# Kernel tuning notes

Measured on AMD Instinct MI355X. Metric: run time of the kernel, lower is better.

Reference implementation:

```python
import jax, jax.numpy as jnp
import numpy as np

B, TQ, TK = 8, 2048, 4096
DIM_IMG, DIM_TXT, HS = 512, 128, 64


def _make_freqs(seqlen, half_dim):
    # standard RoPE angles: theta = pos * 10000^(-2i/d); stored as [T, half_dim, 2] = (cos, sin)
    inv = 1.0 / (10000.0 ** (np.arange(0, half_dim, dtype=np.float32) / half_dim))
    ang = np.arange(seqlen, dtype=np.float32)[:, None] * inv[None, :]
    return jnp.asarray(np.stack([np.cos(ang), np.sin(ang)], axis=-1))


def _rot_complex(x, f):
    # x: [B, T, D]; f: [T, D//2, 2] (real, imag). Complex multiply on (even, odd) pairs.
    xr = x.reshape(*x.shape[:-1], -1, 2)
    a, b = xr[..., 0], xr[..., 1]
    fr, fi = f[None, ..., 0], f[None, ..., 1]
    out = jnp.stack([a * fr - b * fi, a * fi + b * fr], axis=-1)
    return out.reshape(x.shape)


def _rot2d(x, fx, fy):
    vx, vy = jnp.split(x, 2, axis=-1)
    return jnp.concatenate([_rot_complex(vx, fx), _rot_complex(vy, fy)], axis=-1)


def setup_inputs() -> dict:
    key = jax.random.key(0)
    k1, k2, k3, k4, k5 = jax.random.split(key, 5)
    return {
        "x_image": jax.random.normal(k1, (B, TK, DIM_IMG), dtype=jnp.float32),
        "x_text_emb": jax.random.normal(k2, (B, TQ, DIM_TXT), dtype=jnp.float32),
        "x_latex_mask": jax.random.randint(k3, (B, TQ), 0, 2, dtype=jnp.int32),
        "freqs_latex": _make_freqs(TQ, HS // 2),
        "freqs_img_x": _make_freqs(TK, HS // 4),
        "freqs_img_y": _make_freqs(TK, HS // 4),
        "Wk": jax.random.normal(k4, (HS, DIM_IMG), dtype=jnp.float32) * (DIM_IMG ** -0.5),
        "Wq": jax.random.normal(k5, (HS, DIM_TXT), dtype=jnp.float32) * (DIM_TXT ** -0.5),
        "Wv": jax.random.normal(jax.random.fold_in(key, 7), (HS, DIM_IMG), dtype=jnp.float32) * (DIM_IMG ** -0.5),
    }


def reference(x_image, x_text_emb, x_latex_mask, freqs_latex, freqs_img_x, freqs_img_y, Wk, Wq, Wv):
    C = x_image.shape[-1]  # original divides by sqrt of image embed dim (512), not head_size
    k = jnp.einsum("btc,hc->bth", x_image, Wk)
    k = jax.lax.stop_gradient(_rot2d(k, freqs_img_x, freqs_img_y))  # torch.no_grad in source
    q = jnp.einsum("bsc,hc->bsh", x_text_emb, Wq)
    q = jax.lax.stop_gradient(_rot_complex(q, freqs_latex))  # torch.no_grad in source
    v = jnp.einsum("btc,hc->bth", x_image, Wv)
    wei = jnp.einsum("bsh,bth->bst", q, k) / (C ** 0.5)  # [B, TQ, TK]
    softwei = jax.nn.softmax(wei, axis=-1)
    out = jnp.einsum("bst,bth->bsh", softwei, v)
    return out
```

## Files before the change

### kernel.cpp

```cpp
#include <hip/hip_runtime.h>


#define B_    8
#define TQ_   2048
#define TK_   4096
#define DIMG  512
#define DTXT  128
#define HS_   64
#define NSPL  4
#define TSPL  (TK_ / NSPL)

typedef float f32x4 __attribute__((ext_vector_type(4)));
typedef __bf16 bf16x8 __attribute__((ext_vector_type(8)));

static __device__ __forceinline__ unsigned short f2bf(float x) {
    __bf16 b = (__bf16)x;
    return __builtin_bit_cast(unsigned short, b);
}
static __device__ __forceinline__ unsigned pk2(float a, float b) {
    return (unsigned)f2bf(a) | ((unsigned)f2bf(b) << 16);
}

#define STAGE_KV(XBUF, WBUF, kc)                                                      \
    {                                                                                 \
        _Pragma("unroll")                                                             \
        for (int m = 0; m < 4; ++m) {                                                 \
            int lin = tid + 256 * m;                                                  \
            int r = lin >> 4;                                                         \
            int c = (lin & 15) * 4;                                                   \
            float4 v = *(const float4*)(x_image + ((size_t)(b * TK_ + t0 + r)) * DIMG + (kc) + c); \
            *(uint2*)&XBUF[r][c] = make_uint2(pk2(v.x, v.y), pk2(v.z, v.w));          \
        }                                                                             \
        _Pragma("unroll")                                                             \
        for (int m = 0; m < 8; ++m) {                                                 \
            int lin = tid + 256 * m;                                                  \
            int r = lin >> 4;                                                         \
            int c = (lin & 15) * 4;                                                   \
            const float* src = (r < 64) ? (Wk + (size_t)r * DIMG + (kc) + c)          \
                                        : (Wv + (size_t)(r - 64) * DIMG + (kc) + c);  \
            float4 v = *(const float4*)src;                                           \
            *(uint2*)&WBUF[r][c] = make_uint2(pk2(v.x, v.y), pk2(v.z, v.w));          \
        }                                                                             \
    }

#define COMPUTE_KV(XBUF, WBUF)                                                        \
    {                                                                                 \
        bf16x8 a0 = *(const bf16x8*)&XBUF[16 * w + col][hi4 * 8];                     \
        bf16x8 a1 = *(const bf16x8*)&XBUF[16 * w + col][hi4 * 8 + 32];                \
        _Pragma("unroll")                                                             \
        for (int g = 0; g < 8; ++g) {                                                 \
            bf16x8 b0 = *(const bf16x8*)&WBUF[g * 16 + col][hi4 * 8];                 \
            bf16x8 b1 = *(const bf16x8*)&WBUF[g * 16 + col][hi4 * 8 + 32];            \
            acc[g] = __builtin_amdgcn_mfma_f32_16x16x32_bf16(a0, b0, acc[g], 0, 0, 0);\
            acc[g] = __builtin_amdgcn_mfma_f32_16x16x32_bf16(a1, b1, acc[g], 0, 0, 0);\
        }                                                                             \
    }

__global__ __launch_bounds__(256) void proj_fused_kernel(
    const float* __restrict__ x_image, const float* __restrict__ fx,
    const float* __restrict__ fy, const float* __restrict__ Wk,
    const float* __restrict__ Wv, const float* __restrict__ x_text,
    const float* __restrict__ fl, const float* __restrict__ Wq,
    unsigned short* __restrict__ K_ws, unsigned short* __restrict__ Vt_ws,
    unsigned short* __restrict__ Q_ws)
{
    __shared__ __align__(16) unsigned short lds[27648];

    const int tid = threadIdx.x;
    const int bid = blockIdx.x;
    const int w  = tid >> 6;
    const int l  = tid & 63;
    const int col = l & 15;
    const int hi4 = l >> 4;

    if (bid < 512) {
        auto Xc0 = (unsigned short(*)[72])(lds);
        auto Xc1 = (unsigned short(*)[72])(lds + 4608);
        auto Wc0 = (unsigned short(*)[72])(lds + 9216);
        auto Wc1 = (unsigned short(*)[72])(lds + 18432);

        const int b  = bid & 7;
        const int t0 = (bid >> 3) * 64;

        f32x4 acc[8];
        #pragma unroll
        for (int g = 0; g < 8; ++g) acc[g] = (f32x4){0.f, 0.f, 0.f, 0.f};

        STAGE_KV(Xc0, Wc0, 0);
        __syncthreads();
        for (int c2 = 0; c2 < 8; c2 += 2) {
            STAGE_KV(Xc1, Wc1, (c2 + 1) * 64);
            COMPUTE_KV(Xc0, Wc0);
            __syncthreads();
            if (c2 + 2 < 8) STAGE_KV(Xc0, Wc0, (c2 + 2) * 64);
            COMPUTE_KV(Xc1, Wc1);
            __syncthreads();
        }

        const int rbase = hi4 * 4;
        #pragma unroll
        for (int g = 0; g < 4; ++g) {
            int h = g * 16 + col;
            const float* ftab = (h < 32) ? fx : fy;
            int i = (h & 31) >> 1;
            float sgn = (h & 1) ? 1.f : -1.f;
            #pragma unroll
            for (int j = 0; j < 4; ++j) {
                int t = t0 + 16 * w + rbase + j;
                float v = acc[g][j];
                float p = __shfl_xor(v, 1);
                float2 cs = *(const float2*)(ftab + ((size_t)t * 16 + i) * 2);
                float o = v * cs.x + sgn * p * cs.y;
                K_ws[((size_t)(b * TK_ + t)) * HS_ + h] = f2bf(o);
            }
        }
        #pragma unroll
        for (int g = 4; g < 8; ++g) {
            int h = (g - 4) * 16 + col;
            int tb = t0 + 16 * w + rbase;
            *(uint2*)&Vt_ws[((size_t)(b * HS_ + h)) * TK_ + tb] =
                make_uint2(pk2(acc[g][0], acc[g][1]), pk2(acc[g][2], acc[g][3]));
        }
    } else {
        auto Xq = (unsigned short(*)[136])(lds);
        auto Wl = (unsigned short(*)[136])(lds + 8704);

        const int b  = bid & 7;
        const int s0 = ((bid - 512) >> 3) * 64;

        #pragma unroll
        for (int m = 0; m < 8; ++m) {
            int lin = tid + 256 * m;
            int r = lin >> 5;
            int c = (lin & 31) * 4;
            float4 v = *(const float4*)(x_text + ((size_t)(b * TQ_ + s0 + r)) * DTXT + c);
            *(uint2*)&Xq[r][c] = make_uint2(pk2(v.x, v.y), pk2(v.z, v.w));
        }
        #pragma unroll
        for (int m = 0; m < 8; ++m) {
            int lin = tid + 256 * m;
            int r = lin >> 5;
            int c = (lin & 31) * 4;
            float4 v = *(const float4*)(Wq + (size_t)r * DTXT + c);
            *(uint2*)&Wl[r][c] = make_uint2(pk2(v.x, v.y), pk2(v.z, v.w));
        }
        __syncthreads();

        f32x4 acc[4];
        #pragma unroll
        for (int g = 0; g < 4; ++g) acc[g] = (f32x4){0.f, 0.f, 0.f, 0.f};
        #pragma unroll
        for (int kk = 0; kk < 4; ++kk) {
            bf16x8 a = *(const bf16x8*)&Xq[16 * w + col][hi4 * 8 + kk * 32];
            #pragma unroll
            for (int g = 0; g < 4; ++g) {
                bf16x8 bb = *(const bf16x8*)&Wl[g * 16 + col][hi4 * 8 + kk * 32];
                acc[g] = __builtin_amdgcn_mfma_f32_16x16x32_bf16(a, bb, acc[g], 0, 0, 0);
            }
        }

        const float SCALE = 0.044194173824159216f;
        const int rbase = hi4 * 4;
        #pragma unroll
        for (int g = 0; g < 4; ++g) {
            int h = g * 16 + col;
            int i = h >> 1;
            float sgn = (h & 1) ? 1.f : -1.f;
            #pragma unroll
            for (int j = 0; j < 4; ++j) {
                int s = s0 + 16 * w + rbase + j;
                float v = acc[g][j];
                float p = __shfl_xor(v, 1);
                float2 cs = *(const float2*)(fl + ((size_t)s * 32 + i) * 2);
                float o = (v * cs.x + sgn * p * cs.y) * SCALE;
                Q_ws[((size_t)(b * TQ_ + s)) * HS_ + h] = f2bf(o);
            }
        }
    }
}

__global__ __launch_bounds__(512, 4) void attn_partial_kernel(
    const unsigned short* __restrict__ Q_ws,
    const unsigned short* __restrict__ K_ws,
    const unsigned short* __restrict__ Vt_ws,
    float* __restrict__ num_ws, float* __restrict__ den_ws)
{
    __shared__ unsigned short Kt[128][72];
    __shared__ unsigned short Vv[64][136];
    __shared__ unsigned short Pl[8][16][136];

    const int tid  = threadIdx.x;
    const int bid  = blockIdx.x;
    const int b    = bid & 7;
    const int rest = bid >> 3;
    const int stile = rest & 15;
    const int split = rest >> 4;
    const int s0 = stile * 128;
    const int w  = tid >> 6;
    const int l  = tid & 63;
    const int col = l & 15;
    const int hi4 = l >> 4;

    const int srow = s0 + 16 * w + col;
    bf16x8 q0 = *(const bf16x8*)(Q_ws + ((size_t)(b * TQ_ + srow)) * HS_ + hi4 * 8);
    bf16x8 q1 = *(const bf16x8*)(Q_ws + ((size_t)(b * TQ_ + srow)) * HS_ + hi4 * 8 + 32);

    f32x4 oacc[4];
    #pragma unroll
    for (int g = 0; g < 4; ++g) oacc[g] = (f32x4){0.f, 0.f, 0.f, 0.f};
    f32x4 den = (f32x4){0.f, 0.f, 0.f, 0.f};

    const int tbase = split * TSPL;
    const int lin1 = tid + 512;
    const int kr_r0 = tid >> 3,  kr_h0 = (tid & 7) * 8;
    const int kr_r1 = lin1 >> 3, kr_h1 = (lin1 & 7) * 8;
    const int vr_h0 = tid >> 4,  vr_t0 = (tid & 15) * 8;
    const int vr_h1 = lin1 >> 4, vr_t1 = (lin1 & 15) * 8;

    *(uint4*)&Kt[kr_r0][kr_h0] = *(const uint4*)(K_ws + ((size_t)(b * TK_ + tbase + kr_r0)) * HS_ + kr_h0);
    *(uint4*)&Kt[kr_r1][kr_h1] = *(const uint4*)(K_ws + ((size_t)(b * TK_ + tbase + kr_r1)) * HS_ + kr_h1);
    *(uint4*)&Vv[vr_h0][vr_t0] = *(const uint4*)(Vt_ws + ((size_t)(b * HS_ + vr_h0)) * TK_ + tbase + vr_t0);
    *(uint4*)&Vv[vr_h1][vr_t1] = *(const uint4*)(Vt_ws + ((size_t)(b * HS_ + vr_h1)) * TK_ + tbase + vr_t1);
    __syncthreads();

    for (int ti = 0; ti < TSPL / 128; ++ti) {
        const int tt = tbase + ti * 128;
        const bool pre = (ti + 1 < TSPL / 128);
        uint4 kr0, kr1, vr0, vr1;
        if (pre) {
            const int tn = tt + 128;
            kr0 = *(const uint4*)(K_ws + ((size_t)(b * TK_ + tn + kr_r0)) * HS_ + kr_h0);
            kr1 = *(const uint4*)(K_ws + ((size_t)(b * TK_ + tn + kr_r1)) * HS_ + kr_h1);
            vr0 = *(const uint4*)(Vt_ws + ((size_t)(b * HS_ + vr_h0)) * TK_ + tn + vr_t0);
            vr1 = *(const uint4*)(Vt_ws + ((size_t)(b * HS_ + vr_h1)) * TK_ + tn + vr_t1);
        }

        #pragma unroll
        for (int n = 0; n < 8; ++n) {
            bf16x8 k0 = *(const bf16x8*)&Kt[n * 16 + col][hi4 * 8];
            bf16x8 k1 = *(const bf16x8*)&Kt[n * 16 + col][hi4 * 8 + 32];
            f32x4 p = (f32x4){0.f, 0.f, 0.f, 0.f};
            p = __builtin_amdgcn_mfma_f32_16x16x32_bf16(q0, k0, p, 0, 0, 0);
            p = __builtin_amdgcn_mfma_f32_16x16x32_bf16(q1, k1, p, 0, 0, 0);
            #pragma unroll
            for (int j = 0; j < 4; ++j) {
                float e = __expf(p[j]);
                den[j] += e;
                Pl[w][hi4 * 4 + j][n * 16 + col] = f2bf(e);
            }
        }
        asm volatile("s_waitcnt lgkmcnt(0)" ::: "memory");
        __builtin_amdgcn_sched_barrier(0);

        #pragma unroll
        for (int c = 0; c < 4; ++c) {
            bf16x8 pa = *(const bf16x8*)&Pl[w][col][c * 32 + hi4 * 8];
            #pragma unroll
            for (int g = 0; g < 4; ++g) {
                bf16x8 vb = *(const bf16x8*)&Vv[g * 16 + col][c * 32 + hi4 * 8];
                oacc[g] = __builtin_amdgcn_mfma_f32_16x16x32_bf16(pa, vb, oacc[g], 0, 0, 0);
            }
        }
        __syncthreads();
        if (pre) {
            *(uint4*)&Kt[kr_r0][kr_h0] = kr0;
            *(uint4*)&Kt[kr_r1][kr_h1] = kr1;
            *(uint4*)&Vv[vr_h0][vr_t0] = vr0;
            *(uint4*)&Vv[vr_h1][vr_t1] = vr1;
        }
        __syncthreads();
    }

    #pragma unroll
    for (int m = 1; m < 16; m <<= 1) {
        #pragma unroll
        for (int j = 0; j < 4; ++j) den[j] += __shfl_xor(den[j], m);
    }

    const size_t sec = (size_t)(split * B_ + b) * TQ_;
    #pragma unroll
    for (int g = 0; g < 4; ++g) {
        #pragma unroll
        for (int j = 0; j < 4; ++j) {
            int s = s0 + 16 * w + hi4 * 4 + j;
            num_ws[(sec + s) * HS_ + g * 16 + col] = oacc[g][j];
        }
    }
    if (col == 0) {
        #pragma unroll
        for (int j = 0; j < 4; ++j) {
            int s = s0 + 16 * w + hi4 * 4 + j;
            den_ws[sec + s] = den[j];
        }
    }
}

__global__ __launch_bounds__(256) void attn_reduce_kernel(
    const float* __restrict__ num_ws, const float* __restrict__ den_ws,
    float* __restrict__ out)
{
    const int idx = blockIdx.x * 256 + threadIdx.x;
    const int row = idx >> 4;
    const size_t spl4 = (size_t)B_ * TQ_ * HS_ / 4;
    const float4* n4 = (const float4*)num_ws;
    float4 a = n4[idx];
    float4 v1 = n4[idx + spl4];
    float4 v2 = n4[idx + 2 * spl4];
    float4 v3 = n4[idx + 3 * spl4];
    a.x += v1.x + v2.x + v3.x;
    a.y += v1.y + v2.y + v3.y;
    a.z += v1.z + v2.z + v3.z;
    a.w += v1.w + v2.w + v3.w;
    float d = den_ws[row] + den_ws[row + B_ * TQ_] +
              den_ws[row + 2 * B_ * TQ_] + den_ws[row + 3 * B_ * TQ_];
    float inv = 1.f / d;
    a.x *= inv; a.y *= inv; a.z *= inv; a.w *= inv;
    ((float4*)out)[idx] = a;
}

__global__ __launch_bounds__(256) void attn_kernel(
    const unsigned short* __restrict__ Q_ws,
    const unsigned short* __restrict__ K_ws,
    const unsigned short* __restrict__ Vt_ws,
    float* __restrict__ out)
{
    __shared__ unsigned short Kt[128][72];
    __shared__ unsigned short Vv[64][136];
    __shared__ unsigned short Pl[4][16][136];

    const int tid = threadIdx.x;
    const int b  = blockIdx.x & 7;
    const int s0 = (blockIdx.x >> 3) * 64;
    const int w  = tid >> 6;
    const int l  = tid & 63;
    const int col = l & 15;
    const int hi4 = l >> 4;

    const int srow = s0 + 16 * w + col;
    bf16x8 q0 = *(const bf16x8*)(Q_ws + ((size_t)(b * TQ_ + srow)) * HS_ + hi4 * 8);
    bf16x8 q1 = *(const bf16x8*)(Q_ws + ((size_t)(b * TQ_ + srow)) * HS_ + hi4 * 8 + 32);

    f32x4 oacc[4];
    #pragma unroll
    for (int g = 0; g < 4; ++g) oacc[g] = (f32x4){0.f, 0.f, 0.f, 0.f};
    f32x4 den = (f32x4){0.f, 0.f, 0.f, 0.f};

    for (int tt = 0; tt < TK_; tt += 128) {
        #pragma unroll
        for (int m = 0; m < 4; ++m) {
            int lin = tid + 256 * m;
            int r = lin >> 3;
            int h = (lin & 7) * 8;
            *(uint4*)&Kt[r][h] = *(const uint4*)(K_ws + ((size_t)(b * TK_ + tt + r)) * HS_ + h);
        }
        #pragma unroll
        for (int m = 0; m < 4; ++m) {
            int lin = tid + 256 * m;
            int h  = lin >> 4;
            int tk = (lin & 15) * 8;
            *(uint4*)&Vv[h][tk] = *(const uint4*)(Vt_ws + ((size_t)(b * HS_ + h)) * TK_ + tt + tk);
        }
        __syncthreads();

        #pragma unroll
        for (int n = 0; n < 8; ++n) {
            bf16x8 k0 = *(const bf16x8*)&Kt[n * 16 + col][hi4 * 8];
            bf16x8 k1 = *(const bf16x8*)&Kt[n * 16 + col][hi4 * 8 + 32];
            f32x4 p = (f32x4){0.f, 0.f, 0.f, 0.f};
            p = __builtin_amdgcn_mfma_f32_16x16x32_bf16(q0, k0, p, 0, 0, 0);
            p = __builtin_amdgcn_mfma_f32_16x16x32_bf16(q1, k1, p, 0, 0, 0);
            #pragma unroll
            for (int j = 0; j < 4; ++j) {
                float e = __expf(p[j]);
                den[j] += e;
                Pl[w][hi4 * 4 + j][n * 16 + col] = f2bf(e);
            }
        }
        asm volatile("s_waitcnt lgkmcnt(0)" ::: "memory");
        __builtin_amdgcn_sched_barrier(0);

        #pragma unroll
        for (int c = 0; c < 4; ++c) {
            bf16x8 pa = *(const bf16x8*)&Pl[w][col][c * 32 + hi4 * 8];
            #pragma unroll
            for (int g = 0; g < 4; ++g) {
                bf16x8 vb = *(const bf16x8*)&Vv[g * 16 + col][c * 32 + hi4 * 8];
                oacc[g] = __builtin_amdgcn_mfma_f32_16x16x32_bf16(pa, vb, oacc[g], 0, 0, 0);
            }
        }
        __syncthreads();
    }

    #pragma unroll
    for (int m = 1; m < 16; m <<= 1) {
        #pragma unroll
        for (int j = 0; j < 4; ++j) den[j] += __shfl_xor(den[j], m);
    }
    float inv[4];
    #pragma unroll
    for (int j = 0; j < 4; ++j) inv[j] = 1.f / den[j];

    #pragma unroll
    for (int g = 0; g < 4; ++g) {
        #pragma unroll
        for (int j = 0; j < 4; ++j) {
            int s = s0 + 16 * w + hi4 * 4 + j;
            out[((size_t)(b * TQ_ + s)) * HS_ + g * 16 + col] = oacc[g][j] * inv[j];
        }
    }
}

extern "C" void kernel_launch(void* const* d_in, const int* in_sizes, int n_in,
                              void* d_out, int out_size, void* d_ws, size_t ws_size,
                              hipStream_t stream) {
    const float* x_image = (const float*)d_in[0];
    const float* x_text  = (const float*)d_in[1];
    const float* fl      = (const float*)d_in[3];
    const float* fx      = (const float*)d_in[4];
    const float* fy      = (const float*)d_in[5];
    const float* Wk      = (const float*)d_in[6];
    const float* Wq      = (const float*)d_in[7];
    const float* Wv      = (const float*)d_in[8];

    unsigned short* K_ws  = (unsigned short*)d_ws;
    unsigned short* Vt_ws = K_ws + (size_t)B_ * TK_ * HS_;
    unsigned short* Q_ws  = Vt_ws + (size_t)B_ * TK_ * HS_;
    float* out = (float*)d_out;

    const size_t kvq_bytes = (size_t)(2 * B_ * TK_ * HS_ + B_ * TQ_ * HS_) * 2;
    const size_t num_bytes = (size_t)NSPL * B_ * TQ_ * HS_ * 4;
    const size_t den_bytes = (size_t)NSPL * B_ * TQ_ * 4;

    proj_fused_kernel<<<dim3(768), dim3(256), 0, stream>>>(
        x_image, fx, fy, Wk, Wv, x_text, fl, Wq, K_ws, Vt_ws, Q_ws);

    if (ws_size >= kvq_bytes + num_bytes + den_bytes) {
        float* num_ws = (float*)((char*)d_ws + kvq_bytes);
        float* den_ws = num_ws + (size_t)NSPL * B_ * TQ_ * HS_;
        attn_partial_kernel<<<dim3(512), dim3(512), 0, stream>>>(Q_ws, K_ws, Vt_ws, num_ws, den_ws);
        attn_reduce_kernel<<<dim3(B_ * TQ_ * HS_ / 4 / 256), dim3(256), 0, stream>>>(num_ws, den_ws, out);
    } else {
        attn_kernel<<<dim3(256), dim3(256), 0, stream>>>(Q_ws, K_ws, Vt_ws, out);
    }
}
```

Baseline: 158.6 us.

## Load V directly from global into MFMA operands and double key splits

The V tile no longer goes through shared memory. Each lane reads its bf16x8 V operand straight from global (L2) inside the PV loop, which frees LDS and removes the V staging stores. The key dimension is split eight ways instead of four, so the grid doubles to 1024 blocks, the occupancy hint rises to 6, and the reduce kernel loops over NSPL. The trade-off is more partial-sum traffic and global-load latency sitting inside the MFMA loop, in return for higher occupancy and less LDS pressure.

```diff
diff --git a/kernel.cpp b/kernel.cpp
--- a/kernel.cpp
+++ b/kernel.cpp
@@ -7,7 +7,7 @@
 #define DIMG  512
 #define DTXT  128
 #define HS_   64
-#define NSPL  4
+#define NSPL  8
 #define TSPL  (TK_ / NSPL)
 
 typedef float f32x4 __attribute__((ext_vector_type(4)));
@@ -179,14 +179,13 @@
     }
 }
 
-__global__ __launch_bounds__(512, 4) void attn_partial_kernel(
+__global__ __launch_bounds__(512, 6) void attn_partial_kernel(
     const unsigned short* __restrict__ Q_ws,
     const unsigned short* __restrict__ K_ws,
     const unsigned short* __restrict__ Vt_ws,
     float* __restrict__ num_ws, float* __restrict__ den_ws)
 {
     __shared__ unsigned short Kt[128][72];
-    __shared__ unsigned short Vv[64][136];
     __shared__ unsigned short Pl[8][16][136];
 
     const int tid  = threadIdx.x;
@@ -205,6 +204,11 @@
     bf16x8 q0 = *(const bf16x8*)(Q_ws + ((size_t)(b * TQ_ + srow)) * HS_ + hi4 * 8);
     bf16x8 q1 = *(const bf16x8*)(Q_ws + ((size_t)(b * TQ_ + srow)) * HS_ + hi4 * 8 + 32);
 
+    const unsigned short* vb0 = Vt_ws + ((size_t)(b * HS_ +  0 + col)) * TK_ + hi4 * 8;
+    const unsigned short* vb1 = Vt_ws + ((size_t)(b * HS_ + 16 + col)) * TK_ + hi4 * 8;
+    const unsigned short* vb2 = Vt_ws + ((size_t)(b * HS_ + 32 + col)) * TK_ + hi4 * 8;
+    const unsigned short* vb3 = Vt_ws + ((size_t)(b * HS_ + 48 + col)) * TK_ + hi4 * 8;
+
     f32x4 oacc[4];
     #pragma unroll
     for (int g = 0; g < 4; ++g) oacc[g] = (f32x4){0.f, 0.f, 0.f, 0.f};
@@ -214,25 +218,19 @@
     const int lin1 = tid + 512;
     const int kr_r0 = tid >> 3,  kr_h0 = (tid & 7) * 8;
     const int kr_r1 = lin1 >> 3, kr_h1 = (lin1 & 7) * 8;
-    const int vr_h0 = tid >> 4,  vr_t0 = (tid & 15) * 8;
-    const int vr_h1 = lin1 >> 4, vr_t1 = (lin1 & 15) * 8;
 
     *(uint4*)&Kt[kr_r0][kr_h0] = *(const uint4*)(K_ws + ((size_t)(b * TK_ + tbase + kr_r0)) * HS_ + kr_h0);
     *(uint4*)&Kt[kr_r1][kr_h1] = *(const uint4*)(K_ws + ((size_t)(b * TK_ + tbase + kr_r1)) * HS_ + kr_h1);
-    *(uint4*)&Vv[vr_h0][vr_t0] = *(const uint4*)(Vt_ws + ((size_t)(b * HS_ + vr_h0)) * TK_ + tbase + vr_t0);
-    *(uint4*)&Vv[vr_h1][vr_t1] = *(const uint4*)(Vt_ws + ((size_t)(b * HS_ + vr_h1)) * TK_ + tbase + vr_t1);
     __syncthreads();
 
     for (int ti = 0; ti < TSPL / 128; ++ti) {
         const int tt = tbase + ti * 128;
         const bool pre = (ti + 1 < TSPL / 128);
-        uint4 kr0, kr1, vr0, vr1;
+        uint4 kr0, kr1;
         if (pre) {
             const int tn = tt + 128;
             kr0 = *(const uint4*)(K_ws + ((size_t)(b * TK_ + tn + kr_r0)) * HS_ + kr_h0);
             kr1 = *(const uint4*)(K_ws + ((size_t)(b * TK_ + tn + kr_r1)) * HS_ + kr_h1);
-            vr0 = *(const uint4*)(Vt_ws + ((size_t)(b * HS_ + vr_h0)) * TK_ + tn + vr_t0);
-            vr1 = *(const uint4*)(Vt_ws + ((size_t)(b * HS_ + vr_h1)) * TK_ + tn + vr_t1);
         }
 
         #pragma unroll
@@ -255,18 +253,19 @@
         #pragma unroll
         for (int c = 0; c < 4; ++c) {
             bf16x8 pa = *(const bf16x8*)&Pl[w][col][c * 32 + hi4 * 8];
-            #pragma unroll
-            for (int g = 0; g < 4; ++g) {
-                bf16x8 vb = *(const bf16x8*)&Vv[g * 16 + col][c * 32 + hi4 * 8];
-                oacc[g] = __builtin_amdgcn_mfma_f32_16x16x32_bf16(pa, vb, oacc[g], 0, 0, 0);
-            }
+            bf16x8 v0 = *(const bf16x8*)(vb0 + tt + c * 32);
+            bf16x8 v1 = *(const bf16x8*)(vb1 + tt + c * 32);
+            bf16x8 v2 = *(const bf16x8*)(vb2 + tt + c * 32);
+            bf16x8 v3 = *(const bf16x8*)(vb3 + tt + c * 32);
+            oacc[0] = __builtin_amdgcn_mfma_f32_16x16x32_bf16(pa, v0, oacc[0], 0, 0, 0);
+            oacc[1] = __builtin_amdgcn_mfma_f32_16x16x32_bf16(pa, v1, oacc[1], 0, 0, 0);
+            oacc[2] = __builtin_amdgcn_mfma_f32_16x16x32_bf16(pa, v2, oacc[2], 0, 0, 0);
+            oacc[3] = __builtin_amdgcn_mfma_f32_16x16x32_bf16(pa, v3, oacc[3], 0, 0, 0);
         }
         __syncthreads();
         if (pre) {
             *(uint4*)&Kt[kr_r0][kr_h0] = kr0;
             *(uint4*)&Kt[kr_r1][kr_h1] = kr1;
-            *(uint4*)&Vv[vr_h0][vr_t0] = vr0;
-            *(uint4*)&Vv[vr_h1][vr_t1] = vr1;
         }
         __syncthreads();
     }
@@ -304,15 +303,13 @@
     const size_t spl4 = (size_t)B_ * TQ_ * HS_ / 4;
     const float4* n4 = (const float4*)num_ws;
     float4 a = n4[idx];
-    float4 v1 = n4[idx + spl4];
-    float4 v2 = n4[idx + 2 * spl4];
-    float4 v3 = n4[idx + 3 * spl4];
-    a.x += v1.x + v2.x + v3.x;
-    a.y += v1.y + v2.y + v3.y;
-    a.z += v1.z + v2.z + v3.z;
-    a.w += v1.w + v2.w + v3.w;
-    float d = den_ws[row] + den_ws[row + B_ * TQ_] +
-              den_ws[row + 2 * B_ * TQ_] + den_ws[row + 3 * B_ * TQ_];
+    float d = den_ws[row];
+    #pragma unroll
+    for (int k = 1; k < NSPL; ++k) {
+        float4 v = n4[idx + (size_t)k * spl4];
+        a.x += v.x; a.y += v.y; a.z += v.z; a.w += v.w;
+        d += den_ws[row + k * B_ * TQ_];
+    }
     float inv = 1.f / d;
     a.x *= inv; a.y *= inv; a.z *= inv; a.w *= inv;
     ((float4*)out)[idx] = a;
@@ -437,7 +434,7 @@
     if (ws_size >= kvq_bytes + num_bytes + den_bytes) {
         float* num_ws = (float*)((char*)d_ws + kvq_bytes);
         float* den_ws = num_ws + (size_t)NSPL * B_ * TQ_ * HS_;
-        attn_partial_kernel<<<dim3(512), dim3(512), 0, stream>>>(Q_ws, K_ws, Vt_ws, num_ws, den_ws);
+        attn_partial_kernel<<<dim3(1024), dim3(512), 0, stream>>>(Q_ws, K_ws, Vt_ws, num_ws, den_ws);
         attn_reduce_kernel<<<dim3(B_ * TQ_ * HS_ / 4 / 256), dim3(256), 0, stream>>>(num_ws, den_ws, out);
     } else {
         attn_kernel<<<dim3(256), dim3(256), 0, stream>>>(Q_ws, K_ws, Vt_ws, out);
```

Result: slower. 202.9 us (+27.9%).
